# Kernel tuning notes

Hardware: AMD Instinct MI355X
Metric: run time of the kernel (lower is better)

The kernel has to match this reference:

```python
import jax, jax.numpy as jnp
import numpy as np

S, H, A = 8192, 4096, 1024

def setup_inputs() -> dict:
    key = jax.random.key(0)
    ks = jax.random.split(key, 8)
    return {
        "encoder_outputs": jax.random.normal(ks[0], (S, H), jnp.float32),
        "hidden": jax.random.normal(ks[1], (H,), jnp.float32),
        "U_w": jax.random.normal(ks[2], (A, H), jnp.float32) * (1.0 / np.sqrt(H)),
        "U_b": jax.random.normal(ks[3], (A,), jnp.float32) * 0.01,
        "W_w": jax.random.normal(ks[4], (A, H), jnp.float32) * (1.0 / np.sqrt(H)),
        "W_b": jax.random.normal(ks[5], (A,), jnp.float32) * 0.01,
        "V_w": jax.random.normal(ks[6], (1, A), jnp.float32) * (1.0 / np.sqrt(A)),
        "V_b": jax.random.normal(ks[7], (1,), jnp.float32) * 0.01,
    }

def reference(encoder_outputs, hidden, U_w, U_b, W_w, W_b, V_w, V_b):
    # Bahdanau additive attention ('add' mode).
    W_hidden = hidden @ W_w.T + W_b                      # [A]
    U_encode = encoder_outputs @ U_w.T + U_b             # [S, A]
    poly_tanh = jnp.tanh(U_encode + W_hidden)            # [S, A]
    scores = poly_tanh @ V_w.T + V_b                     # [S, 1]
    attn = jax.nn.softmax(scores, axis=0)                # softmax over sequence
    context = attn.T @ encoder_outputs                   # [1, H]
    return context[None]                                 # [1, 1, H] (matches torch bmm)
```

## Files before the change

### kernel.cpp

```cpp
#include <hip/hip_runtime.h>

typedef __attribute__((ext_vector_type(8))) short short8;
typedef __attribute__((ext_vector_type(4))) float f32x4;

#define S_DIM 8192
#define H_DIM 4096
#define A_DIM 1024

__device__ __forceinline__ short f2bf(float x) {
  unsigned u = __float_as_uint(x);
  u += 0x7fffu + ((u >> 16) & 1u);
  return (short)(u >> 16);
}

__device__ __forceinline__ float bf2f(short b) {
  return __uint_as_float(((unsigned)(unsigned short)b) << 16);
}

__device__ __forceinline__ float fast_tanh(float x) {
  float e = __expf(-2.f * fabsf(x));
  float r = __fdividef(1.f - e, 1.f + e);
  return copysignf(r, x);
}

__device__ __forceinline__ void gload16(const void* g, void* l) {
  __builtin_amdgcn_global_load_lds(
      (const __attribute__((address_space(1))) void*)g,
      (__attribute__((address_space(3))) void*)l, 16, 0, 0);
}

__global__ __launch_bounds__(256) void comb_kernel(const float* __restrict__ hidden,
                                                   const float* __restrict__ Ww,
                                                   const float* __restrict__ Wb,
                                                   const float* __restrict__ Ub,
                                                   float* __restrict__ comb) {
  const int wave = threadIdx.x >> 6;
  const int lane = threadIdx.x & 63;
  const int a = blockIdx.x * 4 + wave;
  const float* row = Ww + (size_t)a * H_DIM;
  float acc = 0.f;
  for (int k = lane * 4; k < H_DIM; k += 64 * 4) {
    float4 w = *(const float4*)(row + k);
    float4 h = *(const float4*)(hidden + k);
    acc += w.x * h.x + w.y * h.y + w.z * h.z + w.w * h.w;
  }
  #pragma unroll
  for (int mk = 1; mk < 64; mk <<= 1) acc += __shfl_xor(acc, mk);
  if (lane == 0) comb[a] = acc + Wb[a] + Ub[a];
}

__global__ __launch_bounds__(256) void cvt_kernel(const float* __restrict__ src,
                                                  unsigned short* __restrict__ dst,
                                                  int n8) {
  const int stride = gridDim.x * blockDim.x;
  for (int i = blockIdx.x * blockDim.x + threadIdx.x; i < n8; i += stride) {
    float4 a = ((const float4*)src)[(size_t)i * 2];
    float4 b = ((const float4*)src)[(size_t)i * 2 + 1];
    short8 o;
    o[0] = f2bf(a.x); o[1] = f2bf(a.y); o[2] = f2bf(a.z); o[3] = f2bf(a.w);
    o[4] = f2bf(b.x); o[5] = f2bf(b.y); o[6] = f2bf(b.z); o[7] = f2bf(b.w);
    ((short8*)dst)[i] = o;
  }
}

__global__ __launch_bounds__(128) void gemm_score_f_kernel(
    const unsigned short* __restrict__ A,
    const unsigned short* __restrict__ B,
    const float* __restrict__ comb,
    const float* __restrict__ Vw,
    float* __restrict__ scores) {
  __shared__ __align__(16) unsigned short sA[128 * 64];
  __shared__ __align__(16) unsigned short sB[64 * 64];

  const int tid  = threadIdx.x;
  const int lane = tid & 63;
  const int wave = tid >> 6;
  const int m0 = blockIdx.x * 128;
  const int n0 = blockIdx.y * 64;

  const int scol = (lane & 7) * 8;
  const unsigned short* ga = A + (size_t)(m0 + wave * 64 + (lane >> 3)) * H_DIM + scol;
  const unsigned short* gb = B + (size_t)(n0 + wave * 32 + (lane >> 3)) * H_DIM + scol;

  #define STAGE(kt) do {                                                      \
    const unsigned short* pa_ = ga + (size_t)(kt) * 64;                       \
    const unsigned short* pb_ = gb + (size_t)(kt) * 64;                       \
    _Pragma("unroll")                                                         \
    for (int i_ = 0; i_ < 8; ++i_)                                            \
      gload16(pa_ + (size_t)i_ * 8 * H_DIM, &sA[(wave * 64 + i_ * 8) * 64]);  \
    _Pragma("unroll")                                                         \
    for (int i_ = 0; i_ < 4; ++i_)                                            \
      gload16(pb_ + (size_t)i_ * 8 * H_DIM, &sB[(wave * 32 + i_ * 8) * 64]);  \
  } while (0)

  f32x4 acc[4][4];
  const f32x4 zero = {0.f, 0.f, 0.f, 0.f};
  #pragma unroll
  for (int i = 0; i < 4; ++i)
    #pragma unroll
    for (int j = 0; j < 4; ++j) acc[i][j] = zero;

  STAGE(0);

  const int NK = H_DIM / 64;
  for (int kt = 0; kt < NK; ++kt) {
    __syncthreads();

    short8 af[2][4], bfr[2][4];
    #pragma unroll
    for (int ks = 0; ks < 2; ++ks) {
      #pragma unroll
      for (int i = 0; i < 4; ++i)
        af[ks][i] = *(const short8*)&sA[(wave * 64 + i * 16 + (lane & 15)) * 64 + ks * 32 + (lane >> 4) * 8];
      #pragma unroll
      for (int j = 0; j < 4; ++j)
        bfr[ks][j] = *(const short8*)&sB[(j * 16 + (lane & 15)) * 64 + ks * 32 + (lane >> 4) * 8];
    }
    __syncthreads();

    if (kt + 1 < NK) STAGE(kt + 1);

    #pragma unroll
    for (int ks = 0; ks < 2; ++ks)
      #pragma unroll
      for (int i = 0; i < 4; ++i)
        #pragma unroll
        for (int j = 0; j < 4; ++j)
          acc[i][j] = __builtin_amdgcn_mfma_f32_16x16x32_bf16(af[ks][i], bfr[ks][j], acc[i][j], 0, 0, 0);
  }
  #undef STAGE

  float vwv[4], cbv[4];
  #pragma unroll
  for (int j = 0; j < 4; ++j) {
    const int col = n0 + j * 16 + (lane & 15);
    vwv[j] = Vw[col];
    cbv[j] = comb[col];
  }
  #pragma unroll
  for (int i = 0; i < 4; ++i) {
    #pragma unroll
    for (int r = 0; r < 4; ++r) {
      float s = 0.f;
      #pragma unroll
      for (int j = 0; j < 4; ++j)
        s += vwv[j] * fast_tanh(acc[i][j][r] + cbv[j]);
      s += __shfl_xor(s, 1);
      s += __shfl_xor(s, 2);
      s += __shfl_xor(s, 4);
      s += __shfl_xor(s, 8);
      if ((lane & 15) == 0) {
        const int grow = m0 + wave * 64 + i * 16 + (lane >> 4) * 4 + r;
        atomicAdd(&scores[grow], s);
      }
    }
  }
}

__global__ __launch_bounds__(1024) void softmax_kernel(const float* __restrict__ scores,
                                                       float* __restrict__ attn) {
  __shared__ float redm[16];
  __shared__ float reds[16];
  const int tid = threadIdx.x;
  const int lane = tid & 63, wid = tid >> 6;
  float v[8];
  float m = -3.0e38f;
  #pragma unroll
  for (int i = 0; i < 8; ++i) { v[i] = scores[i * 1024 + tid]; m = fmaxf(m, v[i]); }
  #pragma unroll
  for (int mk = 1; mk < 64; mk <<= 1) m = fmaxf(m, __shfl_xor(m, mk));
  if (lane == 0) redm[wid] = m;
  __syncthreads();
  float M = redm[0];
  #pragma unroll
  for (int j = 1; j < 16; ++j) M = fmaxf(M, redm[j]);
  float e[8]; float s = 0.f;
  #pragma unroll
  for (int i = 0; i < 8; ++i) { e[i] = __expf(v[i] - M); s += e[i]; }
  #pragma unroll
  for (int mk = 1; mk < 64; mk <<= 1) s += __shfl_xor(s, mk);
  if (lane == 0) reds[wid] = s;
  __syncthreads();
  float T = 0.f;
  #pragma unroll
  for (int j = 0; j < 16; ++j) T += reds[j];
  const float inv = 1.f / T;
  #pragma unroll
  for (int i = 0; i < 8; ++i) attn[i * 1024 + tid] = e[i] * inv;
}

__global__ __launch_bounds__(256) void context_bf_kernel(const unsigned short* __restrict__ Ebf,
                                                         const float* __restrict__ attn,
                                                         float* __restrict__ partial) {
  const int h0 = (blockIdx.x * 256 + threadIdx.x) * 8;
  const int s0 = blockIdx.y * 64;
  float acc[8] = {0.f, 0.f, 0.f, 0.f, 0.f, 0.f, 0.f, 0.f};
  for (int s = s0; s < s0 + 64; ++s) {
    const float w = attn[s];
    short8 e = *(const short8*)(Ebf + (size_t)s * H_DIM + h0);
    #pragma unroll
    for (int j = 0; j < 8; ++j) acc[j] += w * bf2f(e[j]);
  }
  float* p = partial + (size_t)blockIdx.y * H_DIM + h0;
  #pragma unroll
  for (int j = 0; j < 8; ++j) p[j] = acc[j];
}

__global__ __launch_bounds__(256) void context_reduce_kernel(const float* __restrict__ partial,
                                                             float* __restrict__ out) {
  const int h = blockIdx.x * 256 + threadIdx.x;
  float acc = 0.f;
  #pragma unroll 8
  for (int y = 0; y < 128; ++y) acc += partial[(size_t)y * H_DIM + h];
  out[h] = acc;
}


#define LDSW 40
__global__ __launch_bounds__(256) void gemm_score_kernel(const float* __restrict__ E,
                                                         const float* __restrict__ Uw,
                                                         const float* __restrict__ comb,
                                                         const float* __restrict__ Vw,
                                                         float* __restrict__ scores) {
  __shared__ __align__(16) short sA[128 * LDSW];
  __shared__ __align__(16) short sB[128 * LDSW];
  const int tid  = threadIdx.x;
  const int lane = tid & 63;
  const int wave = tid >> 6;
  const int wm = wave >> 1, wn = wave & 1;
  const int m0 = blockIdx.x * 128;
  const int n0 = blockIdx.y * 128;
  const int sr = tid >> 1;
  const int sh = tid & 1;
  const float* gA = E  + (size_t)(m0 + sr) * H_DIM + sh * 16;
  const float* gB = Uw + (size_t)(n0 + sr) * H_DIM + sh * 16;
  alignas(16) float fa[16], fb[16];
  #pragma unroll
  for (int j = 0; j < 4; ++j) {
    *(float4*)&fa[j * 4] = *(const float4*)(gA + j * 4);
    *(float4*)&fb[j * 4] = *(const float4*)(gB + j * 4);
  }
  f32x4 acc[4][4];
  const f32x4 zero = {0.f, 0.f, 0.f, 0.f};
  #pragma unroll
  for (int i = 0; i < 4; ++i)
    #pragma unroll
    for (int j = 0; j < 4; ++j) acc[i][j] = zero;
  short* wA = &sA[sr * LDSW + sh * 16];
  short* wB = &sB[sr * LDSW + sh * 16];
  const int NK = H_DIM / 32;
  for (int kt = 0; kt < NK; ++kt) {
    short8 ca0, ca1, cb0, cb1;
    #pragma unroll
    for (int j = 0; j < 8; ++j) {
      ca0[j] = f2bf(fa[j]);     ca1[j] = f2bf(fa[8 + j]);
      cb0[j] = f2bf(fb[j]);     cb1[j] = f2bf(fb[8 + j]);
    }
    __syncthreads();
    *(short8*)(wA)     = ca0;
    *(short8*)(wA + 8) = ca1;
    *(short8*)(wB)     = cb0;
    *(short8*)(wB + 8) = cb1;
    __syncthreads();
    if (kt + 1 < NK) {
      const float* pA = gA + (kt + 1) * 32;
      const float* pB = gB + (kt + 1) * 32;
      #pragma unroll
      for (int j = 0; j < 4; ++j) {
        *(float4*)&fa[j * 4] = *(const float4*)(pA + j * 4);
        *(float4*)&fb[j * 4] = *(const float4*)(pB + j * 4);
      }
    }
    short8 af[4], bfr[4];
    #pragma unroll
    for (int i = 0; i < 4; ++i)
      af[i] = *(const short8*)&sA[(wm * 64 + i * 16 + (lane & 15)) * LDSW + (lane >> 4) * 8];
    #pragma unroll
    for (int j = 0; j < 4; ++j)
      bfr[j] = *(const short8*)&sB[(wn * 64 + j * 16 + (lane & 15)) * LDSW + (lane >> 4) * 8];
    #pragma unroll
    for (int i = 0; i < 4; ++i)
      #pragma unroll
      for (int j = 0; j < 4; ++j)
        acc[i][j] = __builtin_amdgcn_mfma_f32_16x16x32_bf16(af[i], bfr[j], acc[i][j], 0, 0, 0);
  }
  float vwv[4], cbv[4];
  #pragma unroll
  for (int j = 0; j < 4; ++j) {
    const int col = n0 + wn * 64 + j * 16 + (lane & 15);
    vwv[j] = Vw[col];
    cbv[j] = comb[col];
  }
  #pragma unroll
  for (int i = 0; i < 4; ++i) {
    #pragma unroll
    for (int r = 0; r < 4; ++r) {
      float s = 0.f;
      #pragma unroll
      for (int j = 0; j < 4; ++j)
        s += vwv[j] * fast_tanh(acc[i][j][r] + cbv[j]);
      s += __shfl_xor(s, 1);
      s += __shfl_xor(s, 2);
      s += __shfl_xor(s, 4);
      s += __shfl_xor(s, 8);
      if ((lane & 15) == 0) {
        const int grow = m0 + wm * 64 + i * 16 + (lane >> 4) * 4 + r;
        atomicAdd(&scores[grow], s);
      }
    }
  }
}

__global__ __launch_bounds__(256) void context_kernel(const float* __restrict__ E,
                                                      const float* __restrict__ attn,
                                                      float* __restrict__ out) {
  const int h  = blockIdx.x * 256 + threadIdx.x;
  const int s0 = blockIdx.y * 256;
  float acc = 0.f;
  #pragma unroll 4
  for (int s = s0; s < s0 + 256; ++s)
    acc += attn[s] * E[(size_t)s * H_DIM + h];
  atomicAdd(&out[h], acc);
}


extern "C" void kernel_launch(void* const* d_in, const int* in_sizes, int n_in,
                              void* d_out, int out_size, void* d_ws, size_t ws_size,
                              hipStream_t stream) {
  const float* E   = (const float*)d_in[0];
  const float* hid = (const float*)d_in[1];
  const float* Uw  = (const float*)d_in[2];
  const float* Ub  = (const float*)d_in[3];
  const float* Ww  = (const float*)d_in[4];
  const float* Wb  = (const float*)d_in[5];
  const float* Vw  = (const float*)d_in[6];

  float* out    = (float*)d_out;
  float* ws     = (float*)d_ws;
  float* comb   = ws;
  float* scores = ws + 1024;
  float* attn   = ws + 9216;
  float* ctxp   = ws + 17408;
  const size_t CTXP = (size_t)128 * H_DIM;

  unsigned short* Ebf  = (unsigned short*)(ws + 17408 + CTXP);
  unsigned short* Uwbf = Ebf + (size_t)S_DIM * H_DIM;
  const size_t NEED = ((size_t)17408 + CTXP) * 4
                    + ((size_t)S_DIM + A_DIM) * H_DIM * 2;

  hipMemsetAsync(scores, 0, S_DIM * sizeof(float), stream);

  comb_kernel<<<A_DIM / 4, 256, 0, stream>>>(hid, Ww, Wb, Ub, comb);

  if (ws_size >= NEED) {
    cvt_kernel<<<2048, 256, 0, stream>>>(E, Ebf, (int)((size_t)S_DIM * H_DIM / 8));
    cvt_kernel<<<512, 256, 0, stream>>>(Uw, Uwbf, (int)((size_t)A_DIM * H_DIM / 8));

    gemm_score_f_kernel<<<dim3(S_DIM / 128, A_DIM / 64), 128, 0, stream>>>(
        Ebf, Uwbf, comb, Vw, scores);

    softmax_kernel<<<1, 1024, 0, stream>>>(scores, attn);

    context_bf_kernel<<<dim3(H_DIM / 2048, S_DIM / 64), 256, 0, stream>>>(Ebf, attn, ctxp);
    context_reduce_kernel<<<H_DIM / 256, 256, 0, stream>>>(ctxp, out);
  } else {
    hipMemsetAsync(out, 0, (size_t)out_size * sizeof(float), stream);
    gemm_score_kernel<<<dim3(S_DIM / 128, A_DIM / 128), 256, 0, stream>>>(E, Uw, comb, Vw, scores);
    softmax_kernel<<<1, 1024, 0, stream>>>(scores, attn);
    context_kernel<<<dim3(H_DIM / 256, 32), 256, 0, stream>>>(E, attn, out);
  }
}
```

Before: 176.9 us.

## Split GEMM K dimension across wave pairs with XOR-swizzled LDS and LDS reduction

Replaces the 128x64-tile, 2-wave score GEMM with a 64x128-tile, 4-wave kernel in which two wave pairs each handle half of the K range. The pairs then combine their partial accumulators through shared memory before the tanh/V epilogue. Shared-memory tiles now use an XOR-swizzled column layout to reduce bank conflicts on the fragment reads. The aim is more waves per block for latency hiding and fewer LDS conflicts, at the cost of an extra LDS reduction step and half the waves sitting idle during the epilogue.

```diff
diff --git a/kernel.cpp b/kernel.cpp
--- a/kernel.cpp
+++ b/kernel.cpp
@@ -63,34 +63,41 @@
   }
 }
 
-__global__ __launch_bounds__(128) void gemm_score_f_kernel(
+__global__ __launch_bounds__(256) void gemm_wsplit_kernel(
     const unsigned short* __restrict__ A,
     const unsigned short* __restrict__ B,
     const float* __restrict__ comb,
     const float* __restrict__ Vw,
     float* __restrict__ scores) {
-  __shared__ __align__(16) unsigned short sA[128 * 64];
-  __shared__ __align__(16) unsigned short sB[64 * 64];
+  __shared__ __align__(16) unsigned short sA[2][64 * 64];
+  __shared__ __align__(16) unsigned short sB[2][128 * 64];
 
   const int tid  = threadIdx.x;
   const int lane = tid & 63;
   const int wave = tid >> 6;
-  const int m0 = blockIdx.x * 128;
-  const int n0 = blockIdx.y * 64;
-
-  const int scol = (lane & 7) * 8;
-  const unsigned short* ga = A + (size_t)(m0 + wave * 64 + (lane >> 3)) * H_DIM + scol;
-  const unsigned short* gb = B + (size_t)(n0 + wave * 32 + (lane >> 3)) * H_DIM + scol;
+  const int h    = wave >> 1;
+  const int wn   = wave & 1;
+  const int m0 = blockIdx.x * 64;
+  const int n0 = blockIdx.y * 128;
+  const int kbase = h * (H_DIM / 2);
+
+  const int rA  = lane & 15;
+  const int grp = lane >> 4;
+  const int lx  = lane & 7;
+
+  const int permEl = (((lane & 7) ^ (lane >> 3)) * 8);
+  const unsigned short* gA = A + (size_t)(m0 + wn * 32 + (lane >> 3)) * H_DIM + kbase + permEl;
+  const unsigned short* gB = B + (size_t)(n0 + wn * 64 + (lane >> 3)) * H_DIM + kbase + permEl;
 
   #define STAGE(kt) do {                                                      \
-    const unsigned short* pa_ = ga + (size_t)(kt) * 64;                       \
-    const unsigned short* pb_ = gb + (size_t)(kt) * 64;                       \
+    const unsigned short* pa_ = gA + (size_t)(kt) * 64;                       \
+    const unsigned short* pb_ = gB + (size_t)(kt) * 64;                       \
+    _Pragma("unroll")                                                         \
+    for (int i_ = 0; i_ < 4; ++i_)                                            \
+      gload16(pa_ + (size_t)i_ * 8 * H_DIM, &sA[h][(wn * 32 + i_ * 8) * 64]); \
     _Pragma("unroll")                                                         \
     for (int i_ = 0; i_ < 8; ++i_)                                            \
-      gload16(pa_ + (size_t)i_ * 8 * H_DIM, &sA[(wave * 64 + i_ * 8) * 64]);  \
-    _Pragma("unroll")                                                         \
-    for (int i_ = 0; i_ < 4; ++i_)                                            \
-      gload16(pb_ + (size_t)i_ * 8 * H_DIM, &sB[(wave * 32 + i_ * 8) * 64]);  \
+      gload16(pb_ + (size_t)i_ * 8 * H_DIM, &sB[h][(wn * 64 + i_ * 8) * 64]); \
   } while (0)
 
   f32x4 acc[4][4];
@@ -102,8 +109,8 @@
 
   STAGE(0);
 
-  const int NK = H_DIM / 64;
-  for (int kt = 0; kt < NK; ++kt) {
+  const int NT = (H_DIM / 2) / 64;
+  for (int kt = 0; kt < NT; ++kt) {
     __syncthreads();
 
     short8 af[2][4], bfr[2][4];
@@ -111,14 +118,14 @@
     for (int ks = 0; ks < 2; ++ks) {
       #pragma unroll
       for (int i = 0; i < 4; ++i)
-        af[ks][i] = *(const short8*)&sA[(wave * 64 + i * 16 + (lane & 15)) * 64 + ks * 32 + (lane >> 4) * 8];
+        af[ks][i] = *(const short8*)&sA[h][(i * 16 + rA) * 64 + (((ks * 4 + grp) ^ lx) * 8)];
       #pragma unroll
       for (int j = 0; j < 4; ++j)
-        bfr[ks][j] = *(const short8*)&sB[(j * 16 + (lane & 15)) * 64 + ks * 32 + (lane >> 4) * 8];
+        bfr[ks][j] = *(const short8*)&sB[h][(wn * 64 + j * 16 + rA) * 64 + (((ks * 4 + grp) ^ lx) * 8)];
     }
     __syncthreads();
 
-    if (kt + 1 < NK) STAGE(kt + 1);
+    if (kt + 1 < NT) STAGE(kt + 1);
 
     #pragma unroll
     for (int ks = 0; ks < 2; ++ks)
@@ -130,27 +137,49 @@
   }
   #undef STAGE
 
+  __syncthreads();
+  float* fregion = (float*)&sB[0][0];
+  if (h == 1) {
+    float* fr = fregion + wn * 4096;
+    #pragma unroll
+    for (int i = 0; i < 4; ++i)
+      #pragma unroll
+      for (int j = 0; j < 4; ++j) {
+        const int slot = ((i * 4 + j) * 4 + grp) * 16 + rA;
+        *(f32x4*)(fr + slot * 4) = acc[i][j];
+      }
+  }
+  __syncthreads();
+  if (h == 1) return;
+
+  const float* fr = fregion + wn * 4096;
   float vwv[4], cbv[4];
   #pragma unroll
   for (int j = 0; j < 4; ++j) {
-    const int col = n0 + j * 16 + (lane & 15);
+    const int col = n0 + wn * 64 + j * 16 + rA;
     vwv[j] = Vw[col];
     cbv[j] = comb[col];
   }
   #pragma unroll
   for (int i = 0; i < 4; ++i) {
+    f32x4 part[4];
+    #pragma unroll
+    for (int j = 0; j < 4; ++j) {
+      const int slot = ((i * 4 + j) * 4 + grp) * 16 + rA;
+      part[j] = *(const f32x4*)(fr + slot * 4);
+    }
     #pragma unroll
     for (int r = 0; r < 4; ++r) {
       float s = 0.f;
       #pragma unroll
       for (int j = 0; j < 4; ++j)
-        s += vwv[j] * fast_tanh(acc[i][j][r] + cbv[j]);
+        s += vwv[j] * fast_tanh(acc[i][j][r] + part[j][r] + cbv[j]);
       s += __shfl_xor(s, 1);
       s += __shfl_xor(s, 2);
       s += __shfl_xor(s, 4);
       s += __shfl_xor(s, 8);
-      if ((lane & 15) == 0) {
-        const int grow = m0 + wave * 64 + i * 16 + (lane >> 4) * 4 + r;
+      if (rA == 0) {
+        const int grow = m0 + i * 16 + grp * 4 + r;
         atomicAdd(&scores[grow], s);
       }
     }
@@ -356,7 +385,7 @@
     cvt_kernel<<<2048, 256, 0, stream>>>(E, Ebf, (int)((size_t)S_DIM * H_DIM / 8));
     cvt_kernel<<<512, 256, 0, stream>>>(Uw, Uwbf, (int)((size_t)A_DIM * H_DIM / 8));
 
-    gemm_score_f_kernel<<<dim3(S_DIM / 128, A_DIM / 64), 128, 0, stream>>>(
+    gemm_wsplit_kernel<<<dim3(S_DIM / 64, A_DIM / 128), 256, 0, stream>>>(
         Ebf, Uwbf, comb, Vw, scores);
 
     softmax_kernel<<<1, 1024, 0, stream>>>(scores, attn);
```

Result: faster. 159.4 us (-9.9%).
